# Performance work log

Hardware: AMD Instinct MI355X
Metric: run time of the kernel (lower is better)

The kernel has to match this reference:

```python
import jax, jax.numpy as jnp
import numpy as np

TEMP = 0.1  # temperature from __init__
EPS = 1e-8  # torch CosineSimilarity eps
B, C, D = 64, 32, 256


def _cos(a, b):
    # a, b: [..., F] -> [...]; matches torch: dot / max(|a||b|, eps)
    dot = jnp.sum(a * b, axis=-1)
    na = jnp.linalg.norm(a, axis=-1)
    nb = jnp.linalg.norm(b, axis=-1)
    return dot / jnp.maximum(na * nb, EPS)


def setup_inputs() -> dict:
    key = jax.random.key(0)
    k1, k2, k3, k4 = jax.random.split(key, 4)
    children_is = jax.random.normal(k1, (B, C, D), dtype=jnp.float32)
    children_js = jax.random.normal(k2, (B, C, D), dtype=jnp.float32)
    neg_idx_j = jax.random.randint(k3, (B, B, C), 0, C, dtype=jnp.int32)
    neg_idx_k = jax.random.randint(k4, (B, B, C), 0, C, dtype=jnp.int32)
    partnet_ids = jnp.arange(B, dtype=jnp.int64)
    return {"children_is": children_is, "children_js": children_js,
            "neg_idx_j": neg_idx_j, "neg_idx_k": neg_idx_k,
            "partnet_ids": partnet_ids}


def reference(children_is, children_js, neg_idx_j, neg_idx_k, partnet_ids):
    b, c, d = children_is.shape
    flat_i = children_is.reshape(b, c * d)          # anchors [B, C*D]
    flat_j = children_js.reshape(b, c * d)

    # positive: anchor i vs children_js[i]
    pos = _cos(flat_i, flat_j) / TEMP               # [B]

    src = jnp.arange(b)[None, :, None]              # [1, B, 1]
    # negatives gathered from children_js: [B, B, C, D] -> [B, B, C*D]
    g_j = children_js[src, neg_idx_j].reshape(b, b, c * d)
    # negatives gathered from children_is
    g_k = children_is[src, neg_idx_k].reshape(b, b, c * d)

    sim_j = _cos(flat_i[:, None, :], g_j) / TEMP    # [B, B]
    sim_k = _cos(flat_i[:, None, :], g_k) / TEMP    # [B, B]

    eye = jnp.eye(b, dtype=bool)
    neg_inf = jnp.asarray(-jnp.inf, sim_j.dtype)
    sim_j = jnp.where(eye, neg_inf, sim_j)          # drop j == i
    sim_k = jnp.where(eye, neg_inf, sim_k)          # drop k == i

    # CrossEntropy(reduction='sum') with label 0 per anchor:
    # loss_i = -pos_i + logsumexp([pos_i, negatives...])
    logits = jnp.concatenate([pos[:, None], sim_j, sim_k], axis=1)  # [B, 1+2B]
    lse = jax.scipy.special.logsumexp(logits, axis=1)
    loss = jnp.sum(lse - pos)
    return loss / (2 * b)
```

## Files before the change

kernel.cpp:

```cpp
#include <hip/hip_runtime.h>
#include <math.h>

#define BB 64
#define CC 32
#define DD 256
#define TEMP 0.1f
#define EPSC 1e-8f

__device__ __forceinline__ float wave_reduce_sum(float v) {
    #pragma unroll
    for (int off = 32; off > 0; off >>= 1)
        v += __shfl_down(v, off, 64);
    return v;
}

__global__ __launch_bounds__(256) void sim_fused_kernel(
        const float* __restrict__ xis,
        const float* __restrict__ xjs,
        const int* __restrict__ idxj,
        const int* __restrict__ idxk,
        float* __restrict__ pos,
        float* __restrict__ sim_jT,
        float* __restrict__ sim_kT)
{
    __shared__ float sj[CC * DD];
    __shared__ float sk[CC * DD];

    const int m = blockIdx.x;
    const int lane = threadIdx.x & 63;
    const int wave = __builtin_amdgcn_readfirstlane(threadIdx.x >> 6);

    {
        const float4* gj4 = (const float4*)(xjs + (size_t)m * CC * DD);
        const float4* gi4 = (const float4*)(xis + (size_t)m * CC * DD);
        float4* sj4 = (float4*)sj;
        float4* sk4 = (float4*)sk;
        #pragma unroll
        for (int k = 0; k < 8; ++k) {
            sj4[threadIdx.x + k * 256] = gj4[threadIdx.x + k * 256];
            sk4[threadIdx.x + k * 256] = gi4[threadIdx.x + k * 256];
        }
    }
    __syncthreads();

    const int ibase = blockIdx.y * 16 + wave * 4;

    #pragma unroll
    for (int ii = 0; ii < 4; ++ii) {
        const int i = ibase + ii;
        const bool diag = (i == m);
        const int* __restrict__ pj = idxj + ((size_t)i * BB + m) * CC;
        const int* __restrict__ pk = idxk + ((size_t)i * BB + m) * CC;
        const float4* a4 = (const float4*)(xis + (size_t)i * CC * DD);

        float dj = 0.f, dk = 0.f, naa = 0.f, njj = 0.f, nkk = 0.f;
        #pragma unroll 8
        for (int c = 0; c < CC; ++c) {
            const int ij = diag ? c : pj[c];
            const int ik = diag ? c : pk[c];
            float4 a  = a4[c * (DD / 4) + lane];
            float4 jv = ((const float4*)(sj + ij * DD))[lane];
            float4 kv = ((const float4*)(sk + ik * DD))[lane];
            dj  += a.x * jv.x + a.y * jv.y + a.z * jv.z + a.w * jv.w;
            dk  += a.x * kv.x + a.y * kv.y + a.z * kv.z + a.w * kv.w;
            naa += a.x * a.x  + a.y * a.y  + a.z * a.z  + a.w * a.w;
            njj += jv.x * jv.x + jv.y * jv.y + jv.z * jv.z + jv.w * jv.w;
            nkk += kv.x * kv.x + kv.y * kv.y + kv.z * kv.z + kv.w * kv.w;
        }
        dj  = wave_reduce_sum(dj);
        dk  = wave_reduce_sum(dk);
        naa = wave_reduce_sum(naa);
        njj = wave_reduce_sum(njj);
        nkk = wave_reduce_sum(nkk);

        if (lane == 0) {
            const float ni = sqrtf(naa);
            if (diag) {
                pos[i] = dj / fmaxf(ni * sqrtf(njj), EPSC) / TEMP;
                sim_jT[m * BB + i] = -INFINITY;
                sim_kT[m * BB + i] = -INFINITY;
            } else {
                sim_jT[m * BB + i] = dj / fmaxf(ni * sqrtf(njj), EPSC) / TEMP;
                sim_kT[m * BB + i] = dk / fmaxf(ni * sqrtf(nkk), EPSC) / TEMP;
            }
        }
    }
}

__global__ __launch_bounds__(256) void loss_kernel(
        const float* __restrict__ pos,
        const float* __restrict__ sim_jT,
        const float* __restrict__ sim_kT,
        float* __restrict__ out)
{
    __shared__ float sp[4][BB];
    const int t = threadIdx.x;
    const int i = t & 63;
    const int q = t >> 6;

    float s = 0.f;
    #pragma unroll 4
    for (int mm = 0; mm < 16; ++mm) {
        const int m = q * 16 + mm;
        s += expf(sim_jT[m * BB + i] - 10.0f);
        s += expf(sim_kT[m * BB + i] - 10.0f);
    }
    sp[q][i] = s;
    __syncthreads();

    if (t < 64) {
        const float p = pos[i];
        float tot = sp[0][i] + sp[1][i] + sp[2][i] + sp[3][i] + expf(p - 10.0f);
        float v = 10.0f + logf(tot) - p;
        v = wave_reduce_sum(v);
        if (i == 0) out[0] = v * (1.0f / (2.0f * BB));
    }
}

extern "C" void kernel_launch(void* const* d_in, const int* in_sizes, int n_in,
                              void* d_out, int out_size, void* d_ws, size_t ws_size,
                              hipStream_t stream) {
    const float* xis  = (const float*)d_in[0];
    const float* xjs  = (const float*)d_in[1];
    const int*   idxj = (const int*)d_in[2];
    const int*   idxk = (const int*)d_in[3];
    float* out = (float*)d_out;

    float* ws     = (float*)d_ws;
    float* pos    = ws;
    float* sim_jT = pos + BB;
    float* sim_kT = sim_jT + BB * BB;

    sim_fused_kernel<<<dim3(BB, 4), 256, 0, stream>>>(xis, xjs, idxj, idxk,
                                                      pos, sim_jT, sim_kT);
    loss_kernel<<<1, 256, 0, stream>>>(pos, sim_jT, sim_kT, out);
}
```

Before: 86.44 us.

## Use direct global-to-LDS loads, double grid, and fuse exp into sim kernel

Stages the per-block children tiles into LDS with the global_load_lds builtin when the compiler provides it, instead of loading through registers. It doubles the grid in the y dimension (each wave now handles 2 anchors instead of 4) to raise parallelism across CUs. The exp of both similarities is computed and summed in the first kernel, so only one partial-sum array is written and the loss kernel just adds it up. The grid change also doubles the number of times each block fills LDS with the same 64 KB tile, and the builtin path depends on the toolchain.

After: 77.60 us. 1.11x faster.

```diff
diff --git a/kernel.cpp b/kernel.cpp
--- a/kernel.cpp
+++ b/kernel.cpp
@@ -7,6 +7,9 @@
 #define TEMP 0.1f
 #define EPSC 1e-8f
 
+typedef const __attribute__((address_space(1))) unsigned int* gptr_u32;
+typedef __attribute__((address_space(3))) unsigned int* lptr_u32;
+
 __device__ __forceinline__ float wave_reduce_sum(float v) {
     #pragma unroll
     for (int off = 32; off > 0; off >>= 1)
@@ -14,14 +17,13 @@
     return v;
 }
 
-__global__ __launch_bounds__(256) void sim_fused_kernel(
+__global__ __launch_bounds__(256) void sim_part_kernel(
         const float* __restrict__ xis,
         const float* __restrict__ xjs,
         const int* __restrict__ idxj,
         const int* __restrict__ idxk,
         float* __restrict__ pos,
-        float* __restrict__ sim_jT,
-        float* __restrict__ sim_kT)
+        float* __restrict__ part)
 {
     __shared__ float sj[CC * DD];
     __shared__ float sk[CC * DD];
@@ -31,8 +33,18 @@
     const int wave = __builtin_amdgcn_readfirstlane(threadIdx.x >> 6);
 
     {
-        const float4* gj4 = (const float4*)(xjs + (size_t)m * CC * DD);
-        const float4* gi4 = (const float4*)(xis + (size_t)m * CC * DD);
+        const float* gj = xjs + (size_t)m * CC * DD;
+        const float* gi = xis + (size_t)m * CC * DD;
+#if defined(__has_builtin) && __has_builtin(__builtin_amdgcn_global_load_lds)
+        #pragma unroll
+        for (int k = 0; k < 8; ++k) {
+            const int off = (threadIdx.x + k * 256) * 4;
+            __builtin_amdgcn_global_load_lds((gptr_u32)(gj + off), (lptr_u32)(sj + off), 16, 0, 0);
+            __builtin_amdgcn_global_load_lds((gptr_u32)(gi + off), (lptr_u32)(sk + off), 16, 0, 0);
+        }
+#else
+        const float4* gj4 = (const float4*)gj;
+        const float4* gi4 = (const float4*)gi;
         float4* sj4 = (float4*)sj;
         float4* sk4 = (float4*)sk;
         #pragma unroll
@@ -40,13 +52,14 @@
             sj4[threadIdx.x + k * 256] = gj4[threadIdx.x + k * 256];
             sk4[threadIdx.x + k * 256] = gi4[threadIdx.x + k * 256];
         }
+#endif
     }
     __syncthreads();
 
-    const int ibase = blockIdx.y * 16 + wave * 4;
+    const int ibase = blockIdx.y * 8 + wave * 2;
 
     #pragma unroll
-    for (int ii = 0; ii < 4; ++ii) {
+    for (int ii = 0; ii < 2; ++ii) {
         const int i = ibase + ii;
         const bool diag = (i == m);
         const int* __restrict__ pj = idxj + ((size_t)i * BB + m) * CC;
@@ -77,11 +90,11 @@
             const float ni = sqrtf(naa);
             if (diag) {
                 pos[i] = dj / fmaxf(ni * sqrtf(njj), EPSC) / TEMP;
-                sim_jT[m * BB + i] = -INFINITY;
-                sim_kT[m * BB + i] = -INFINITY;
+                part[m * BB + i] = 0.0f;
             } else {
-                sim_jT[m * BB + i] = dj / fmaxf(ni * sqrtf(njj), EPSC) / TEMP;
-                sim_kT[m * BB + i] = dk / fmaxf(ni * sqrtf(nkk), EPSC) / TEMP;
+                const float s1 = dj / fmaxf(ni * sqrtf(njj), EPSC) / TEMP;
+                const float s2 = dk / fmaxf(ni * sqrtf(nkk), EPSC) / TEMP;
+                part[m * BB + i] = expf(s1 - 10.0f) + expf(s2 - 10.0f);
             }
         }
     }
@@ -89,8 +102,7 @@
 
 __global__ __launch_bounds__(256) void loss_kernel(
         const float* __restrict__ pos,
-        const float* __restrict__ sim_jT,
-        const float* __restrict__ sim_kT,
+        const float* __restrict__ part,
         float* __restrict__ out)
 {
     __shared__ float sp[4][BB];
@@ -99,18 +111,15 @@
     const int q = t >> 6;
 
     float s = 0.f;
-    #pragma unroll 4
-    for (int mm = 0; mm < 16; ++mm) {
-        const int m = q * 16 + mm;
-        s += expf(sim_jT[m * BB + i] - 10.0f);
-        s += expf(sim_kT[m * BB + i] - 10.0f);
-    }
+    #pragma unroll
+    for (int mm = 0; mm < 16; ++mm)
+        s += part[(q * 16 + mm) * BB + i];
     sp[q][i] = s;
     __syncthreads();
 
     if (t < 64) {
         const float p = pos[i];
-        float tot = sp[0][i] + sp[1][i] + sp[2][i] + sp[3][i] + expf(p - 10.0f);
+        const float tot = sp[0][i] + sp[1][i] + sp[2][i] + sp[3][i] + expf(p - 10.0f);
         float v = 10.0f + logf(tot) - p;
         v = wave_reduce_sum(v);
         if (i == 0) out[0] = v * (1.0f / (2.0f * BB));
@@ -126,12 +135,10 @@
     const int*   idxk = (const int*)d_in[3];
     float* out = (float*)d_out;
 
-    float* ws     = (float*)d_ws;
-    float* pos    = ws;
-    float* sim_jT = pos + BB;
-    float* sim_kT = sim_jT + BB * BB;
+    float* ws   = (float*)d_ws;
+    float* pos  = ws;
+    float* part = pos + BB;
 
-    sim_fused_kernel<<<dim3(BB, 4), 256, 0, stream>>>(xis, xjs, idxj, idxk,
-                                                      pos, sim_jT, sim_kT);
-    loss_kernel<<<1, 256, 0, stream>>>(pos, sim_jT, sim_kT, out);
+    sim_part_kernel<<<dim3(BB, 8), 256, 0, stream>>>(xis, xjs, idxj, idxk, pos, part);
+    loss_kernel<<<1, 256, 0, stream>>>(pos, part, out);
 }
```
